# Kernel optimization log

Hardware: AMD Instinct MI355X
Metric: run time of the kernel (lower is better)

Reference implementation:

```python
import jax, jax.numpy as jnp
import numpy as np

N_HEADS = 8
HIDDEN = 256
D_HEAD = HIDDEN // N_HEADS
N_NODES = 4096
N_EDGES = 16384


def setup_inputs() -> dict:
    key = jax.random.key(0)
    ks = jax.random.split(key, 12)
    s = 0.05
    return {
        "q": jax.random.normal(ks[0], (N_EDGES, HIDDEN), jnp.float32),
        "k": jax.random.normal(ks[1], (N_NODES, HIDDEN), jnp.float32),
        "v": jax.random.normal(ks[2], (N_NODES, HIDDEN), jnp.float32),
        "T": jax.random.uniform(ks[3], (N_NODES, N_EDGES), jnp.float32),
        "Wq": jax.random.normal(ks[4], (HIDDEN, HIDDEN), jnp.float32) * s,
        "bq": jax.random.normal(ks[5], (HIDDEN,), jnp.float32) * s,
        "Wk": jax.random.normal(ks[6], (HIDDEN, HIDDEN), jnp.float32) * s,
        "bk": jax.random.normal(ks[7], (HIDDEN,), jnp.float32) * s,
        "Wv": jax.random.normal(ks[8], (HIDDEN, HIDDEN), jnp.float32) * s,
        "bv": jax.random.normal(ks[9], (HIDDEN,), jnp.float32) * s,
        "Wo": jax.random.normal(ks[10], (HIDDEN, HIDDEN), jnp.float32) * s,
        "bo": jax.random.normal(ks[11], (HIDDEN,), jnp.float32) * s,
    }


def reference(q, k, v, T, Wq, bq, Wk, bk, Wv, bv, Wo, bo):
    scale = D_HEAD ** (-0.5)
    # projections, reshaped to per-head layout
    qh = (q @ Wq.T + bq).reshape(-1, N_HEADS, D_HEAD)  # [E, H, d]
    kh = (k @ Wk.T + bk).reshape(-1, N_HEADS, D_HEAD)  # [N, H, d]
    vh = (v @ Wv.T + bv).reshape(-1, N_HEADS, D_HEAD)  # [N, H, d]
    # row-normalized transition matrix (rows with zero sum left unscaled)
    row_sum = jnp.sum(T, axis=-1, keepdims=True)       # [N, 1]
    Tn = T / jnp.where(row_sum == 0, 1.0, row_sum)     # [N, E]
    # edge->node aggregation of queries, then scale
    qn = jnp.einsum("ne,ehd->nhd", Tn, qh) * scale     # [N, H, d]
    # attention: full NxN scores per head
    scores = jnp.einsum("nhd,mhd->hnm", qn, kh)        # [H, N, N]
    attn = jax.nn.softmax(scores, axis=-1)
    ctx = jnp.einsum("hnm,mhd->nhd", attn, vh)         # [N, H, d]
    out = ctx.reshape(-1, N_HEADS * D_HEAD) @ Wo.T + bo  # [N, hidden]
    return out
```

## Files before the change

kernel.cpp:

```cpp
#include <hip/hip_runtime.h>


#define N_NODES 4096
#define N_EDGES 16384
#define HIDDEN  256
#define KSPLIT  16

typedef __attribute__((ext_vector_type(4))) float f32x4;
typedef __attribute__((ext_vector_type(8))) short s16x8;
typedef __attribute__((ext_vector_type(4))) unsigned short u16x4;
typedef __attribute__((ext_vector_type(8))) unsigned short u16x8;

__device__ __forceinline__ unsigned short f2bf(float f) {
    union { float f; unsigned u; } x; x.f = f;
    unsigned r = x.u + 0x7FFFu + ((x.u >> 16) & 1u);
    return (unsigned short)(r >> 16);
}
__device__ __forceinline__ float bf2f(unsigned short u) {
    union { unsigned u; float f; } x; x.u = (unsigned)u << 16; return x.f;
}
__device__ __forceinline__ s16x8 pack8s(f32x4 x, f32x4 y) {
    u16x8 o;
    o[0]=f2bf(x[0]); o[1]=f2bf(x[1]); o[2]=f2bf(x[2]); o[3]=f2bf(x[3]);
    o[4]=f2bf(y[0]); o[5]=f2bf(y[1]); o[6]=f2bf(y[2]); o[7]=f2bf(y[3]);
    union { u16x8 u; s16x8 s; } c; c.u = o; return c.s;
}

__global__ __launch_bounds__(256)
void cvtW(const float* __restrict__ Wq, const float* __restrict__ Wk,
          const float* __restrict__ Wv, const float* __restrict__ Wo,
          unsigned short* __restrict__ dst)
{
    const int g = blockIdx.x * 256 + threadIdx.x;
    const long base = (long)g * 8;
    const int mat = (int)(base >> 16), off = (int)(base & 65535);
    const float* src = (mat == 0) ? Wq : (mat == 1) ? Wk : (mat == 2) ? Wv : Wo;
    f32x4 x = *(const f32x4*)&src[off];
    f32x4 y = *(const f32x4*)&src[off + 4];
    union { u16x8 u; s16x8 s; } c; c.s = pack8s(x, y);
    *(u16x8*)&dst[base] = c.u;
}

template<int MODE>
__global__ __launch_bounds__(256)
void proj_mfma(const float* __restrict__ A, const unsigned short* __restrict__ Wbf,
               const float* __restrict__ bias, unsigned short* __restrict__ out, int M)
{
    const int t = threadIdx.x;
    const int w = t >> 6, l = t & 63, lo = l & 15, h4 = l >> 4;
    const int m0 = blockIdx.x * 64 + w * 16;
    const int bn = blockIdx.y * 64;
    const float* Ar = A + (long)(m0 + lo) * 256 + h4 * 8;

    f32x4 acc[4] = {};
    #pragma unroll
    for (int kk = 0; kk < 8; ++kk) {
        f32x4 x = *(const f32x4*)&Ar[kk * 32];
        f32x4 y = *(const f32x4*)&Ar[kk * 32 + 4];
        s16x8 af = pack8s(x, y);
        #pragma unroll
        for (int nj = 0; nj < 4; ++nj) {
            s16x8 bf = *(const s16x8*)&Wbf[(bn + nj * 16 + lo) * 256 + kk * 32 + h4 * 8];
            acc[nj] = __builtin_amdgcn_mfma_f32_16x16x32_bf16(af, bf, acc[nj], 0, 0, 0);
        }
    }
    #pragma unroll
    for (int nj = 0; nj < 4; ++nj) {
        const int n = bn + nj * 16 + lo;
        const float bi = bias[n];
        if (MODE == 1) {
            #pragma unroll
            for (int r = 0; r < 4; ++r)
                out[(long)(m0 + h4 * 4 + r) * 256 + n] = f2bf(acc[nj][r] + bi);
        } else {
            u16x4 o;
            #pragma unroll
            for (int r = 0; r < 4; ++r) o[r] = f2bf(acc[nj][r] + bi);
            *(u16x4*)&out[(long)n * M + m0 + h4 * 4] = o;
        }
    }
}

__global__ __launch_bounds__(256)
void proj_out_mfma(const float* __restrict__ pctx, const float* __restrict__ plp,
                   const unsigned short* __restrict__ Wobf, const float* __restrict__ bo,
                   float* __restrict__ out)
{
    const int t = threadIdx.x;
    const int w = t >> 6, l = t & 63, lo = l & 15, h4 = l >> 4;
    const int m0 = blockIdx.x * 64 + w * 16;
    const int bn = blockIdx.y * 64;
    const int m = m0 + lo;

    float inv[8];
    #pragma unroll
    for (int h = 0; h < 8; ++h) {
        float s = plp[(0 * 8 + h) * N_NODES + m] + plp[(1 * 8 + h) * N_NODES + m]
                + plp[(2 * 8 + h) * N_NODES + m] + plp[(3 * 8 + h) * N_NODES + m];
        inv[h] = 1.0f / s;
    }
    const float* P = pctx + (long)m * 256;
    const long PS = (long)N_NODES * 256;

    f32x4 acc[4] = {};
    #pragma unroll
    for (int kk = 0; kk < 8; ++kk) {
        const int off = kk * 32 + h4 * 8;
        f32x4 x = *(const f32x4*)&P[off]          + *(const f32x4*)&P[PS + off]
                + *(const f32x4*)&P[2 * PS + off] + *(const f32x4*)&P[3 * PS + off];
        f32x4 y = *(const f32x4*)&P[off + 4]          + *(const f32x4*)&P[PS + off + 4]
                + *(const f32x4*)&P[2 * PS + off + 4] + *(const f32x4*)&P[3 * PS + off + 4];
        s16x8 af = pack8s(x * inv[kk], y * inv[kk]);
        #pragma unroll
        for (int nj = 0; nj < 4; ++nj) {
            s16x8 bf = *(const s16x8*)&Wobf[(bn + nj * 16 + lo) * 256 + kk * 32 + h4 * 8];
            acc[nj] = __builtin_amdgcn_mfma_f32_16x16x32_bf16(af, bf, acc[nj], 0, 0, 0);
        }
    }
    #pragma unroll
    for (int nj = 0; nj < 4; ++nj) {
        const int n = bn + nj * 16 + lo;
        const float bi = bo[n];
        #pragma unroll
        for (int r = 0; r < 4; ++r)
            out[(long)(m0 + h4 * 4 + r) * 256 + n] = acc[nj][r] + bi;
    }
}

__global__ __launch_bounds__(512, 4)
void tgemm(const float* __restrict__ T, const unsigned short* __restrict__ Bt,
           unsigned short* __restrict__ part, float* __restrict__ rsp)
{
    __shared__ __align__(16) unsigned short Bsm[2][256 * 64];
    const int t  = threadIdx.x;
    const int ks = blockIdx.x & 15, ms = blockIdx.x >> 4;
    const int m0 = ms * 128;
    const long k00 = (long)ks * 1024;
    const int w = t >> 6, l = t & 63, lo = l & 15, h4 = l >> 4;

    const int kx = ((l & 7) * 8) ^ ((l >> 3) << 3);
    const unsigned short* Bsrc = Bt + k00 + kx;

#define STAGE(itv, bufv) do {                                                       \
    const unsigned short* _s = Bsrc + (long)(itv) * 64;                             \
    unsigned short* _d = &Bsm[(bufv)][w * 2048];                                    \
    _Pragma("unroll")                                                               \
    for (int _i = 0; _i < 4; ++_i)                                                  \
        __builtin_amdgcn_global_load_lds(                                           \
            (const __attribute__((address_space(1))) unsigned int*)                 \
                (_s + (long)(w * 32 + _i * 8 + (l >> 3)) * N_EDGES),                \
            (__attribute__((address_space(3))) unsigned int*)(_d + _i * 512),       \
            16, 0, 0);                                                              \
} while (0)

    const float* Arow = T + (long)(m0 + w * 16 + lo) * N_EDGES + k00 + h4 * 8;

    f32x4 a0 = *(const f32x4*)&Arow[0];
    f32x4 a1 = *(const f32x4*)&Arow[4];
    f32x4 a2 = *(const f32x4*)&Arow[32];
    f32x4 a3 = *(const f32x4*)&Arow[36];
    STAGE(0, 0);

    f32x4 acc[16] = {};
    float rs = 0.f;

    for (int it = 0; it < 16; ++it) {
        const int cur = it & 1;
        __builtin_amdgcn_s_barrier();
        if (it < 15) {
            STAGE(it + 1, cur ^ 1);
            asm volatile("s_waitcnt vmcnt(4)" ::: "memory");
        } else {
            asm volatile("s_waitcnt vmcnt(0)" ::: "memory");
        }
        s16x8 af0 = pack8s(a0, a1);
        s16x8 af1 = pack8s(a2, a3);
        rs += a0[0]+a0[1]+a0[2]+a0[3] + a1[0]+a1[1]+a1[2]+a1[3]
            + a2[0]+a2[1]+a2[2]+a2[3] + a3[0]+a3[1]+a3[2]+a3[3];
        if (it < 15) {
            const float* An = Arow + (it + 1) * 64;
            a0 = *(const f32x4*)&An[0];
            a1 = *(const f32x4*)&An[4];
            a2 = *(const f32x4*)&An[32];
            a3 = *(const f32x4*)&An[36];
        }
        __builtin_amdgcn_s_barrier();
        __builtin_amdgcn_sched_barrier(0);

        const unsigned short* Bb = Bsm[cur];
        const int swz = (lo & 7) << 3;
        #pragma unroll
        for (int nj = 0; nj < 16; ++nj) {
            const int jb = (nj * 16 + lo) * 64;
            s16x8 bf0 = *(const s16x8*)&Bb[jb + ((h4 * 8) ^ swz)];
            s16x8 bf1 = *(const s16x8*)&Bb[jb + ((32 + h4 * 8) ^ swz)];
            acc[nj] = __builtin_amdgcn_mfma_f32_16x16x32_bf16(af0, bf0, acc[nj], 0, 0, 0);
            acc[nj] = __builtin_amdgcn_mfma_f32_16x16x32_bf16(af1, bf1, acc[nj], 0, 0, 0);
        }
    }
#undef STAGE

    rs += __shfl_xor(rs, 16); rs += __shfl_xor(rs, 32);
    if (h4 == 0) rsp[ks * N_NODES + m0 + w * 16 + lo] = rs;

    unsigned short* P = part + (long)ks * (N_NODES * HIDDEN);
    #pragma unroll
    for (int nj = 0; nj < 16; ++nj)
        #pragma unroll
        for (int r = 0; r < 4; ++r)
            P[(long)(m0 + w * 16 + h4 * 4 + r) * HIDDEN + nj * 16 + lo] = f2bf(acc[nj][r]);
}

__global__ __launch_bounds__(256)
void finalize(const unsigned short* __restrict__ part, const float* __restrict__ rsp,
              unsigned short* __restrict__ qn)
{
    const int idx = blockIdx.x * 256 + threadIdx.x;
    const long i4 = (long)idx * 4;
    const int n = (int)(i4 >> 8);
    f32x4 s = {};
    #pragma unroll
    for (int ksp = 0; ksp < KSPLIT; ++ksp) {
        u16x4 p = *(const u16x4*)&part[(long)ksp * (N_NODES * HIDDEN) + i4];
        #pragma unroll
        for (int i = 0; i < 4; ++i) s[i] += bf2f(p[i]);
    }
    float rs = 0.f;
    #pragma unroll
    for (int ksp = 0; ksp < KSPLIT; ++ksp) rs += rsp[ksp * N_NODES + n];
    rs = (rs == 0.0f) ? 1.0f : rs;
    const float sc = 0.17677669529663687f / rs;
    u16x4 o;
    #pragma unroll
    for (int i = 0; i < 4; ++i) o[i] = f2bf(s[i] * sc);
    *(u16x4*)&qn[i4] = o;
}

__global__ __launch_bounds__(256)
void attn(const unsigned short* __restrict__ qn, const unsigned short* __restrict__ kh,
          const unsigned short* __restrict__ vht, float* __restrict__ pctx,
          float* __restrict__ plp)
{
    __shared__ __align__(16) unsigned short Ksm[64 * 40];
    __shared__ __align__(16) unsigned short Vsm[32 * 72];
    __shared__ __align__(16) unsigned short Psm[4][32 * 72];
    const int t  = threadIdx.x;
    const int hh = blockIdx.x >> 7, nb = (blockIdx.x >> 2) & 31, mh = blockIdx.x & 3;
    const int w = t >> 6, l = t & 63, lo = l & 15, h4 = l >> 4;
    const int n0 = nb * 128 + w * 32;

    const int km = t >> 2, kdc = (t & 3) * 8;
    const int vd = t >> 3, vmc = (t & 7) * 8;

    s16x8 qf[2];
    #pragma unroll
    for (int ni = 0; ni < 2; ++ni)
        qf[ni] = *(const s16x8*)&qn[(long)(n0 + ni * 16 + lo) * HIDDEN + hh * 32 + h4 * 8];

    f32x4 acc[2][2] = {};
    float lp[2][4] = {};
    const f32x4 zero = {};

    for (int mt = mh * 16; mt < mh * 16 + 16; ++mt) {
        const int m0 = mt * 64;
        *(s16x8*)&Ksm[km * 40 + kdc] =
            *(const s16x8*)&kh[(long)(m0 + km) * HIDDEN + hh * 32 + kdc];
        *(s16x8*)&Vsm[vd * 72 + vmc] =
            *(const s16x8*)&vht[(long)(hh * 32 + vd) * N_NODES + m0 + vmc];
        __syncthreads();

        s16x8 kb[4];
        #pragma unroll
        for (int mi = 0; mi < 4; ++mi)
            kb[mi] = *(const s16x8*)&Ksm[(mi * 16 + lo) * 40 + h4 * 8];
        #pragma unroll
        for (int ni = 0; ni < 2; ++ni) {
            #pragma unroll
            for (int mi = 0; mi < 4; ++mi) {
                f32x4 s = __builtin_amdgcn_mfma_f32_16x16x32_bf16(qf[ni], kb[mi], zero, 0, 0, 0);
                #pragma unroll
                for (int r = 0; r < 4; ++r) {
                    float p = __expf(s[r]);
                    lp[ni][r] += p;
                    Psm[w][(ni * 16 + h4 * 4 + r) * 72 + mi * 16 + lo] = f2bf(p);
                }
            }
        }
        s16x8 pa[2][2], vb[2][2];
        #pragma unroll
        for (int ni = 0; ni < 2; ++ni)
            #pragma unroll
            for (int k2 = 0; k2 < 2; ++k2)
                pa[ni][k2] = *(const s16x8*)&Psm[w][(ni * 16 + lo) * 72 + k2 * 32 + h4 * 8];
        #pragma unroll
        for (int di = 0; di < 2; ++di)
            #pragma unroll
            for (int k2 = 0; k2 < 2; ++k2)
                vb[di][k2] = *(const s16x8*)&Vsm[(di * 16 + lo) * 72 + k2 * 32 + h4 * 8];
        #pragma unroll
        for (int k2 = 0; k2 < 2; ++k2)
            #pragma unroll
            for (int ni = 0; ni < 2; ++ni)
                #pragma unroll
                for (int di = 0; di < 2; ++di)
                    acc[ni][di] = __builtin_amdgcn_mfma_f32_16x16x32_bf16(
                        pa[ni][k2], vb[di][k2], acc[ni][di], 0, 0, 0);
        __syncthreads();
    }
    #pragma unroll
    for (int ni = 0; ni < 2; ++ni)
        #pragma unroll
        for (int r = 0; r < 4; ++r) {
            float v2 = lp[ni][r];
            v2 += __shfl_xor(v2, 1); v2 += __shfl_xor(v2, 2);
            v2 += __shfl_xor(v2, 4); v2 += __shfl_xor(v2, 8);
            lp[ni][r] = v2;
        }
    float* myctx = pctx + (long)mh * (N_NODES * HIDDEN);
    float* myplp = plp  + (long)(mh * 8 + hh) * N_NODES;
    if (lo == 0)
        #pragma unroll
        for (int ni = 0; ni < 2; ++ni)
            #pragma unroll
            for (int r = 0; r < 4; ++r)
                myplp[n0 + ni * 16 + h4 * 4 + r] = lp[ni][r];
    #pragma unroll
    for (int ni = 0; ni < 2; ++ni)
        #pragma unroll
        for (int di = 0; di < 2; ++di)
            #pragma unroll
            for (int r = 0; r < 4; ++r)
                myctx[(long)(n0 + ni * 16 + h4 * 4 + r) * HIDDEN + hh * 32 + di * 16 + lo]
                    = acc[ni][di][r];
}

extern "C" void kernel_launch(void* const* d_in, const int* in_sizes, int n_in,
                              void* d_out, int out_size, void* d_ws, size_t ws_size,
                              hipStream_t stream)
{
    const float* q  = (const float*)d_in[0];
    const float* k  = (const float*)d_in[1];
    const float* v  = (const float*)d_in[2];
    const float* T  = (const float*)d_in[3];
    const float* Wq = (const float*)d_in[4];  const float* bq = (const float*)d_in[5];
    const float* Wk = (const float*)d_in[6];  const float* bk = (const float*)d_in[7];
    const float* Wv = (const float*)d_in[8];  const float* bv = (const float*)d_in[9];
    const float* Wo = (const float*)d_in[10]; const float* bo = (const float*)d_in[11];

    char* w = (char*)d_ws;
    unsigned short* qh_t = (unsigned short*)(w);
    unsigned short* kh   = (unsigned short*)(w + (8u  << 20));
    unsigned short* vh_t = (unsigned short*)(w + (10u << 20));
    unsigned short* qn   = (unsigned short*)(w + (12u << 20));
    float*          pctx = (float*)         (w + (14u << 20));
    float*          plp  = (float*)         (w + (30u << 20));
    unsigned short* part = (unsigned short*)(w + (32u << 20));
    float*          rsp  = (float*)         (w + (64u << 20));
    unsigned short* wbf  = (unsigned short*)(w + (65u << 20));
    unsigned short* wq_bf = wbf;
    unsigned short* wk_bf = wbf + 65536;
    unsigned short* wv_bf = wbf + 2 * 65536;
    unsigned short* wo_bf = wbf + 3 * 65536;

    cvtW<<<128, 256, 0, stream>>>(Wq, Wk, Wv, Wo, wbf);
    proj_mfma<2><<<dim3(256, 4), 256, 0, stream>>>(q, wq_bf, bq, qh_t, N_EDGES);
    proj_mfma<1><<<dim3(64, 4),  256, 0, stream>>>(k, wk_bf, bk, kh,   N_NODES);
    proj_mfma<2><<<dim3(64, 4),  256, 0, stream>>>(v, wv_bf, bv, vh_t, N_NODES);
    tgemm<<<512, 512, 0, stream>>>(T, qh_t, part, rsp);
    finalize<<<1024, 256, 0, stream>>>(part, rsp, qn);
    attn<<<1024, 256, 0, stream>>>(qn, kh, vh_t, pctx, plp);
    proj_out_mfma<<<dim3(64, 4), 256, 0, stream>>>(pctx, plp, wo_bf, bo, (float*)d_out);
}
```

Baseline: 201.1 us.

## Store attention partials in bf16, prefetch K/V tiles, pack exp outputs

```diff
diff --git a/kernel.cpp b/kernel.cpp
--- a/kernel.cpp
+++ b/kernel.cpp
@@ -82,7 +82,7 @@
 }
 
 __global__ __launch_bounds__(256)
-void proj_out_mfma(const float* __restrict__ pctx, const float* __restrict__ plp,
+void proj_out_mfma(const unsigned short* __restrict__ pctx, const float* __restrict__ plp,
                    const unsigned short* __restrict__ Wobf, const float* __restrict__ bo,
                    float* __restrict__ out)
 {
@@ -99,17 +99,20 @@
                 + plp[(2 * 8 + h) * N_NODES + m] + plp[(3 * 8 + h) * N_NODES + m];
         inv[h] = 1.0f / s;
     }
-    const float* P = pctx + (long)m * 256;
+    const unsigned short* P = pctx + (long)m * 256;
     const long PS = (long)N_NODES * 256;
 
     f32x4 acc[4] = {};
     #pragma unroll
     for (int kk = 0; kk < 8; ++kk) {
         const int off = kk * 32 + h4 * 8;
-        f32x4 x = *(const f32x4*)&P[off]          + *(const f32x4*)&P[PS + off]
-                + *(const f32x4*)&P[2 * PS + off] + *(const f32x4*)&P[3 * PS + off];
-        f32x4 y = *(const f32x4*)&P[off + 4]          + *(const f32x4*)&P[PS + off + 4]
-                + *(const f32x4*)&P[2 * PS + off + 4] + *(const f32x4*)&P[3 * PS + off + 4];
+        f32x4 x = {}, y = {};
+        #pragma unroll
+        for (int p = 0; p < 4; ++p) {
+            u16x8 v = *(const u16x8*)&P[p * PS + off];
+            #pragma unroll
+            for (int i = 0; i < 4; ++i) { x[i] += bf2f(v[i]); y[i] += bf2f(v[i + 4]); }
+        }
         s16x8 af = pack8s(x * inv[kk], y * inv[kk]);
         #pragma unroll
         for (int nj = 0; nj < 4; ++nj) {
@@ -238,7 +241,7 @@
 
 __global__ __launch_bounds__(256)
 void attn(const unsigned short* __restrict__ qn, const unsigned short* __restrict__ kh,
-          const unsigned short* __restrict__ vht, float* __restrict__ pctx,
+          const unsigned short* __restrict__ vht, unsigned short* __restrict__ pctx,
           float* __restrict__ plp)
 {
     __shared__ __align__(16) unsigned short Ksm[64 * 40];
@@ -257,17 +260,23 @@
     for (int ni = 0; ni < 2; ++ni)
         qf[ni] = *(const s16x8*)&qn[(long)(n0 + ni * 16 + lo) * HIDDEN + hh * 32 + h4 * 8];
 
+    const unsigned short* kp = &kh[(long)(mh * 1024 + km) * HIDDEN + hh * 32 + kdc];
+    const unsigned short* vp = &vht[(long)(hh * 32 + vd) * N_NODES + mh * 1024 + vmc];
+    s16x8 kreg = *(const s16x8*)kp;
+    s16x8 vreg = *(const s16x8*)vp;
+
     f32x4 acc[2][2] = {};
     float lp[2][4] = {};
     const f32x4 zero = {};
 
-    for (int mt = mh * 16; mt < mh * 16 + 16; ++mt) {
-        const int m0 = mt * 64;
-        *(s16x8*)&Ksm[km * 40 + kdc] =
-            *(const s16x8*)&kh[(long)(m0 + km) * HIDDEN + hh * 32 + kdc];
-        *(s16x8*)&Vsm[vd * 72 + vmc] =
-            *(const s16x8*)&vht[(long)(hh * 32 + vd) * N_NODES + m0 + vmc];
+    for (int it = 0; it < 16; ++it) {
+        *(s16x8*)&Ksm[km * 40 + kdc] = kreg;
+        *(s16x8*)&Vsm[vd * 72 + vmc] = vreg;
         __syncthreads();
+        if (it < 15) {
+            kreg = *(const s16x8*)(kp + (long)(it + 1) * 64 * HIDDEN);
+            vreg = *(const s16x8*)(vp + (it + 1) * 64);
+        }
 
         s16x8 kb[4];
         #pragma unroll
@@ -278,12 +287,17 @@
             #pragma unroll
             for (int mi = 0; mi < 4; ++mi) {
                 f32x4 s = __builtin_amdgcn_mfma_f32_16x16x32_bf16(qf[ni], kb[mi], zero, 0, 0, 0);
-                #pragma unroll
-                for (int r = 0; r < 4; ++r) {
-                    float p = __expf(s[r]);
-                    lp[ni][r] += p;
-                    Psm[w][(ni * 16 + h4 * 4 + r) * 72 + mi * 16 + lo] = f2bf(p);
-                }
+                float p0 = __expf(s[0]), p1 = __expf(s[1]);
+                float p2 = __expf(s[2]), p3 = __expf(s[3]);
+                lp[ni][0] += p0; lp[ni][1] += p1; lp[ni][2] += p2; lp[ni][3] += p3;
+                unsigned pk01, pk23;
+                asm("v_cvt_pk_bf16_f32 %0, %1, %2" : "=v"(pk01) : "v"(p0), "v"(p1));
+                asm("v_cvt_pk_bf16_f32 %0, %1, %2" : "=v"(pk23) : "v"(p2), "v"(p3));
+                const int pb = (ni * 16 + h4 * 4) * 72 + mi * 16 + lo;
+                Psm[w][pb]           = (unsigned short)(pk01 & 0xffffu);
+                Psm[w][pb + 72]      = (unsigned short)(pk01 >> 16);
+                Psm[w][pb + 144]     = (unsigned short)(pk23 & 0xffffu);
+                Psm[w][pb + 216]     = (unsigned short)(pk23 >> 16);
             }
         }
         s16x8 pa[2][2], vb[2][2];
@@ -316,7 +330,7 @@
             v2 += __shfl_xor(v2, 4); v2 += __shfl_xor(v2, 8);
             lp[ni][r] = v2;
         }
-    float* myctx = pctx + (long)mh * (N_NODES * HIDDEN);
+    unsigned short* myctx = pctx + (long)mh * (N_NODES * HIDDEN);
     float* myplp = plp  + (long)(mh * 8 + hh) * N_NODES;
     if (lo == 0)
         #pragma unroll
@@ -331,7 +345,7 @@
             #pragma unroll
             for (int r = 0; r < 4; ++r)
                 myctx[(long)(n0 + ni * 16 + h4 * 4 + r) * HIDDEN + hh * 32 + di * 16 + lo]
-                    = acc[ni][di][r];
+                    = f2bf(acc[ni][di][r]);
 }
 
 extern "C" void kernel_launch(void* const* d_in, const int* in_sizes, int n_in,
@@ -352,11 +366,11 @@
     unsigned short* kh   = (unsigned short*)(w + (8u  << 20));
     unsigned short* vh_t = (unsigned short*)(w + (10u << 20));
     unsigned short* qn   = (unsigned short*)(w + (12u << 20));
-    float*          pctx = (float*)         (w + (14u << 20));
-    float*          plp  = (float*)         (w + (30u << 20));
-    unsigned short* part = (unsigned short*)(w + (32u << 20));
-    float*          rsp  = (float*)         (w + (64u << 20));
-    unsigned short* wbf  = (unsigned short*)(w + (65u << 20));
+    unsigned short* pctx = (unsigned short*)(w + (14u << 20));
+    float*          plp  = (float*)         (w + (22u << 20));
+    unsigned short* part = (unsigned short*)(w + (23u << 20));
+    float*          rsp  = (float*)         (w + (55u << 20));
+    unsigned short* wbf  = (unsigned short*)(w + (56u << 20));
     unsigned short* wq_bf = wbf;
     unsigned short* wk_bf = wbf + 65536;
     unsigned short* wv_bf = wbf + 2 * 65536;
```

New measurement: 190.6 us. -5.2%, faster.
